# Kernel optimization log

Hardware: AMD Instinct MI355X
Metric: run time of the kernel (lower is better)

## Reference

```python
import jax, jax.numpy as jnp
import numpy as np
import math

# SS2D (VMamba v2) config
D_MODEL = 96
D_INNER = 192          # ssm_ratio * d_model (== d_expand, ssm_rank_ratio==ssm_ratio)
D_STATE = 16
DT_RANK = 6            # ceil(96/16)
K = 4                  # scan directions
D_CONV = 3
STEP = 2               # EfficientScan step_size
BATCH, H, W = 4, 64, 64  # H,W chosen even -> no padding branch
LN_EPS = 1e-5


def efficient_scan(x):
    # x: (B, C, H, W) with H,W divisible by STEP -> (B, 4, C, (H/2)*(W/2))
    Bn, C = x.shape[0], x.shape[1]
    xt = jnp.swapaxes(x, 2, 3)  # (B, C, W, H)
    xs0 = x[:, :, ::STEP, ::STEP].reshape(Bn, C, -1)
    xs1 = xt[:, :, ::STEP, 1::STEP].reshape(Bn, C, -1)
    xs2 = x[:, :, ::STEP, 1::STEP].reshape(Bn, C, -1)
    xs3 = xt[:, :, 1::STEP, 1::STEP].reshape(Bn, C, -1)
    return jnp.stack([xs0, xs1, xs2, xs3], axis=1)


def efficient_merge(ys, ori_h, ori_w):
    # ys: (B, 4, C, L') -> (B, C, ori_h*ori_w)
    Bn, _, C, _ = ys.shape
    Hs, Ws = ori_h // STEP, ori_w // STEP
    a = ys[:, 0].reshape(Bn, C, Hs, Ws)
    b = jnp.swapaxes(ys[:, 1].reshape(Bn, C, Ws, Hs), 2, 3)
    c = ys[:, 2].reshape(Bn, C, Hs, Ws)
    d = jnp.swapaxes(ys[:, 3].reshape(Bn, C, Ws, Hs), 2, 3)
    y = jnp.zeros((Bn, C, ori_h, ori_w), ys.dtype)
    y = y.at[:, :, ::STEP, ::STEP].set(a)
    y = y.at[:, :, 1::STEP, ::STEP].set(b)
    y = y.at[:, :, ::STEP, 1::STEP].set(c)
    y = y.at[:, :, 1::STEP, 1::STEP].set(d)
    return y.reshape(Bn, C, ori_h * ori_w)


def selective_scan(u, delta, A, Bs, Cs, D, delta_bias):
    # u, delta: (B, K*Dg, L); A: (K*Dg, N); Bs, Cs: (B, K, N, L); D, delta_bias: (K*Dg,)
    Bn, KD, L = u.shape
    N = A.shape[1]
    Dg = KD // K
    delta = jax.nn.softplus(delta + delta_bias[None, :, None])
    u4 = u.reshape(Bn, K, Dg, L)
    dt4 = delta.reshape(Bn, K, Dg, L)
    A4 = A.reshape(K, Dg, N)
    # discretized transition / input, time-major for scan: (L, B, K, Dg, N)
    dA = jnp.exp(jnp.einsum('bkdl,kdn->lbkdn', dt4, A4))
    dBu = jnp.einsum('bkdl,bknl,bkdl->lbkdn', dt4, Bs, u4)

    def step(h, inp):
        dA_t, dBu_t = inp
        h = dA_t * h + dBu_t
        return h, h

    h0 = jnp.zeros((Bn, K, Dg, N), u.dtype)
    _, hs = jax.lax.scan(step, h0, (dA, dBu))  # (L, B, K, Dg, N)
    y = jnp.einsum('lbkdn,bknl->bkdl', hs, Cs)
    y = y + u4 * D.reshape(1, K, Dg, 1)
    return y.reshape(Bn, KD, L)


def setup_inputs() -> dict:
    key = jax.random.key(0)
    ks = jax.random.split(key, 10)
    f = jnp.float32
    x = jax.random.normal(ks[0], (BATCH, H, W, D_MODEL), f)
    W_in = jax.random.normal(ks[1], (2 * D_INNER, D_MODEL), f) / math.sqrt(D_MODEL)
    conv_w = jax.random.normal(ks[2], (D_INNER, 1, D_CONV, D_CONV), f) / math.sqrt(D_CONV * D_CONV)
    conv_b = jax.random.normal(ks[3], (D_INNER,), f) * 0.01
    x_proj_weight = jax.random.normal(ks[4], (K, DT_RANK + 2 * D_STATE, D_INNER), f) / math.sqrt(D_INNER)
    dt_projs_weight = jax.random.normal(ks[5], (K, D_INNER, DT_RANK), f) / math.sqrt(DT_RANK)
    dt_projs_bias = jax.random.normal(ks[6], (K, D_INNER), f) * 0.1
    A_logs = jnp.log(jnp.tile(jnp.arange(1, D_STATE + 1, dtype=f), (K * D_INNER, 1)))
    Ds = jnp.ones((K * D_INNER,), f)
    ln_g = jnp.ones((D_INNER,), f)
    ln_b = jnp.zeros((D_INNER,), f)
    W_out = jax.random.normal(ks[7], (D_MODEL, D_INNER), f) / math.sqrt(D_INNER)
    return dict(x=x, W_in=W_in, conv_w=conv_w, conv_b=conv_b,
                x_proj_weight=x_proj_weight, dt_projs_weight=dt_projs_weight,
                dt_projs_bias=dt_projs_bias, A_logs=A_logs, Ds=Ds,
                ln_g=ln_g, ln_b=ln_b, W_out=W_out)


def _ss2d_forward(x, W_in, conv_w, conv_b, x_proj_weight, dt_projs_weight,
                  dt_projs_bias, A_logs, Ds, ln_g, ln_b, W_out):
    Bn = x.shape[0]
    # in_proj (no bias), split into x and gate z
    xz = jnp.einsum('bhwc,ec->bhwe', x, W_in)            # (B,H,W,2*D_INNER)
    xin, z = jnp.split(xz, 2, axis=-1)
    z = jax.nn.silu(z)
    # depthwise conv 3x3 (SAME) + SiLU, NCHW
    xc = jnp.transpose(xin, (0, 3, 1, 2))                 # (B, D_INNER, H, W)
    xc = jax.lax.conv_general_dilated(
        xc, conv_w, window_strides=(1, 1), padding=((1, 1), (1, 1)),
        feature_group_count=D_INNER,
        dimension_numbers=('NCHW', 'OIHW', 'NCHW')) + conv_b[None, :, None, None]
    xc = jax.nn.silu(xc)
    # cross_selective_scan
    xs = efficient_scan(xc)                               # (B, 4, C, L')
    Lp = xs.shape[-1]
    x_dbl = jnp.einsum('bkdl,kcd->bkcl', xs, x_proj_weight)
    dts, Bs, Cs = jnp.split(x_dbl, [DT_RANK, DT_RANK + D_STATE], axis=2)
    dts = jnp.einsum('bkrl,kdr->bkdl', dts, dt_projs_weight)
    u = xs.reshape(Bn, -1, Lp).astype(jnp.float32)
    delta = dts.reshape(Bn, -1, Lp).astype(jnp.float32)
    A = -jnp.exp(A_logs.astype(jnp.float32))
    ys = selective_scan(u, delta, A, Bs.astype(jnp.float32), Cs.astype(jnp.float32),
                        Ds.astype(jnp.float32), dt_projs_bias.reshape(-1).astype(jnp.float32))
    ys = ys.reshape(Bn, K, -1, Lp)
    y = efficient_merge(ys, H, W)                         # (B, C, H*W)
    y = jnp.swapaxes(y, 1, 2)                             # (B, L, C)
    # LayerNorm over channel dim
    mu = jnp.mean(y, axis=-1, keepdims=True)
    var = jnp.var(y, axis=-1, keepdims=True)
    y = (y - mu) * jax.lax.rsqrt(var + LN_EPS) * ln_g + ln_b
    y = y.reshape(Bn, H, W, D_INNER).astype(x.dtype)
    # gate and out_proj (no bias)
    y = y * z
    out = jnp.einsum('bhwd,od->bhwo', y, W_out)
    return out


def reference(x, W_in, conv_w, conv_b, x_proj_weight, dt_projs_weight,
              dt_projs_bias, A_logs, Ds, ln_g, ln_b, W_out):
    return _ss2d_forward(x, W_in, conv_w, conv_b, x_proj_weight, dt_projs_weight,
                         dt_projs_bias, A_logs, Ds, ln_g, ln_b, W_out)
```

## Files before the change

### kernel.cpp

```cpp
#include <hip/hip_runtime.h>
#include <math.h>


#define DINNER 192
#define NSTATE 16
#define KDIR 4
#define BATCH 4
#define NPIX (BATCH * 64 * 64)
#define LP 1024
#define NCH 64
#define CHUNK 16
#define NBK (BATCH * KDIR)
#define NSTATES (NBK * DINNER * NSTATE)
#define SSTRIDE (NBK * DINNER)
#define USTRIDE 196
#define GSTRIDE 200
#define ASTRIDE 104
#define XSTRIDE 200

typedef __attribute__((ext_vector_type(8))) short short8;
typedef __attribute__((ext_vector_type(4))) short short4v;
typedef __attribute__((ext_vector_type(4))) unsigned short ushort4v;
typedef __attribute__((ext_vector_type(8))) unsigned short ushort8v;
typedef __attribute__((ext_vector_type(4))) float f32x4;

__device__ __forceinline__ float silu_f(float x) {
    return x / (1.0f + __expf(-x));
}
__device__ __forceinline__ float softplus_f(float a) {
    return (a > 20.0f) ? a : __logf(1.0f + __expf(a));
}
__device__ __forceinline__ unsigned short f2bf(float f) {
    unsigned u = __float_as_uint(f);
    unsigned r = (u + 0x7FFFu + ((u >> 16) & 1u)) >> 16;
    return (unsigned short)r;
}
__device__ __forceinline__ float bf2f(unsigned short h) {
    return __uint_as_float(((unsigned)h) << 16);
}

__global__ __launch_bounds__(256) void k_castW(
        const float* __restrict__ W_in, const float* __restrict__ xpw,
        const float* __restrict__ W_out,
        unsigned short* __restrict__ Wi_hi, unsigned short* __restrict__ Wi_lo,
        unsigned short* __restrict__ Xp_hi, unsigned short* __restrict__ Xp_lo,
        unsigned short* __restrict__ Wo_bf) {
    int i = blockIdx.x * 256 + threadIdx.x;
    if (i < 384 * 96) {
        float v = W_in[i];
        unsigned short h = f2bf(v);
        Wi_hi[i] = h;
        Wi_lo[i] = f2bf(v - bf2f(h));
    }
    if (i < 4 * 48 * 192) {
        int kk = i / (48 * 192);
        int rem = i - kk * (48 * 192);
        int c = rem / 192;
        int j = rem - c * 192;
        float v = (c < 38) ? xpw[((size_t)kk * 38 + c) * 192 + j] : 0.0f;
        unsigned short h = f2bf(v);
        Xp_hi[i] = h;
        Xp_lo[i] = f2bf(v - bf2f(h));
    }
    if (i < 96 * DINNER) Wo_bf[i] = f2bf(W_out[i]);
}

__global__ __launch_bounds__(256) void k_inproj3(
        const float* __restrict__ x,
        const unsigned short* __restrict__ Wi_hi,
        const unsigned short* __restrict__ Wi_lo,
        float* __restrict__ xin, unsigned short* __restrict__ zb) {
    __shared__ __align__(16) short sAh[16 * ASTRIDE];
    __shared__ __align__(16) short sAl[16 * ASTRIDE];
    int p0 = blockIdx.x * 16;
    int t = threadIdx.x;
    const float4* xs = (const float4*)(x + (size_t)p0 * 96);
    for (int i = t; i < 384; i += 256) {
        float4 v = xs[i];
        int f = i * 4;
        int row = f / 96, col = f - row * 96;
        short4v hi, lo;
        unsigned short hb;
        hb = f2bf(v.x); hi.x = (short)hb; lo.x = (short)f2bf(v.x - bf2f(hb));
        hb = f2bf(v.y); hi.y = (short)hb; lo.y = (short)f2bf(v.y - bf2f(hb));
        hb = f2bf(v.z); hi.z = (short)hb; lo.z = (short)f2bf(v.z - bf2f(hb));
        hb = f2bf(v.w); hi.w = (short)hb; lo.w = (short)f2bf(v.w - bf2f(hb));
        *(short4v*)&sAh[row * ASTRIDE + col] = hi;
        *(short4v*)&sAl[row * ASTRIDE + col] = lo;
    }
    __syncthreads();
    int w = t >> 6;
    int lane = t & 63;
    int m = lane & 15, quad = lane >> 4;
    const short* wh = (const short*)Wi_hi;
    const short* wl = (const short*)Wi_lo;
    short8 ah[3], al[3];
    #pragma unroll
    for (int c = 0; c < 3; ++c) {
        ah[c] = *(const short8*)&sAh[m * ASTRIDE + c * 32 + quad * 8];
        al[c] = *(const short8*)&sAl[m * ASTRIDE + c * 32 + quad * 8];
    }
    #pragma unroll
    for (int i = 0; i < 6; ++i) {
        int e0 = (w * 6 + i) * 16;
        f32x4 acc = {0.f, 0.f, 0.f, 0.f};
        #pragma unroll
        for (int c = 0; c < 3; ++c) {
            size_t o = (size_t)(e0 + m) * 96 + c * 32 + quad * 8;
            short8 bh = *(const short8*)(wh + o);
            short8 bl = *(const short8*)(wl + o);
            acc = __builtin_amdgcn_mfma_f32_16x16x32_bf16(ah[c], bl, acc, 0, 0, 0);
            acc = __builtin_amdgcn_mfma_f32_16x16x32_bf16(al[c], bh, acc, 0, 0, 0);
            acc = __builtin_amdgcn_mfma_f32_16x16x32_bf16(ah[c], bh, acc, 0, 0, 0);
        }
        int e = e0 + m;
        #pragma unroll
        for (int r = 0; r < 4; ++r) {
            int p = p0 + quad * 4 + r;
            if (e < 192) xin[(size_t)p * 192 + e] = acc[r];
            else         zb[(size_t)p * 192 + (e - 192)] = f2bf(silu_f(acc[r]));
        }
    }
}

__global__ __launch_bounds__(192) void k_conv8(
        const float* __restrict__ xin, const float* __restrict__ cw,
        const float* __restrict__ cb, float* __restrict__ xg) {
    int blk = blockIdx.x;
    int b = blk >> 9;
    int rem = blk & 511;
    int h = rem >> 3;
    int w0 = (rem & 7) * 8;
    int d = threadIdx.x;
    float wr[3][3];
    #pragma unroll
    for (int i = 0; i < 3; ++i)
        #pragma unroll
        for (int j = 0; j < 3; ++j) wr[i][j] = cw[d * 9 + i * 3 + j];
    float bias = cb[d];
    float r0[10], r1[10], r2[10];
    #pragma unroll
    for (int jj = 0; jj < 10; ++jj) {
        int ww = w0 + jj - 1;
        bool inw = (unsigned)ww < 64u;
        const float* base = xin + ((size_t)b * 4096 + h * 64 + (inw ? ww : 0)) * 192 + d;
        r0[jj] = (inw && h > 0)  ? base[-64 * 192] : 0.0f;
        r1[jj] = inw             ? base[0]         : 0.0f;
        r2[jj] = (inw && h < 63) ? base[64 * 192]  : 0.0f;
    }
    float acc[8];
    #pragma unroll
    for (int o = 0; o < 8; ++o) {
        float a = bias;
        #pragma unroll
        for (int j = 0; j < 3; ++j) {
            a = fmaf(r0[o + j], wr[0][j], a);
            a = fmaf(r1[o + j], wr[1][j], a);
            a = fmaf(r2[o + j], wr[2][j], a);
        }
        acc[o] = a;
    }
    #pragma unroll
    for (int o = 0; o < 8; ++o) {
        int w = w0 + o;
        int kq = (h & 1) ? ((w & 1) ? 3 : 1) : ((w & 1) ? 2 : 0);
        int l = (kq & 1) ? ((w >> 1) * 32 + (h >> 1))
                         : ((h >> 1) * 32 + (w >> 1));
        xg[((size_t)(b * 4 + kq) * 1024 + l) * 192 + d] = silu_f(acc[o]);
    }
}

__global__ __launch_bounds__(192) void k_xscan(
        const float* __restrict__ xg,
        const unsigned short* __restrict__ Xp_hi,
        const unsigned short* __restrict__ Xp_lo,
        const float* __restrict__ A_logs, const float* __restrict__ dtw,
        const float* __restrict__ dtb, const float* __restrict__ Ds,
        float* __restrict__ dtr, float* __restrict__ Cm,
        float* __restrict__ Sbuf, unsigned short* __restrict__ Qb,
        unsigned short* __restrict__ yout) {
    __shared__ __align__(16) short sAh[16 * XSTRIDE];
    __shared__ __align__(16) short sAl[16 * XSTRIDE];
    __shared__ __align__(16) float sU[CHUNK * USTRIDE];
    __shared__ float sB[CHUNK * 16];
    __shared__ float sC[CHUNK * 16];
    __shared__ float sDt[CHUNK * 6];

    int bk = blockIdx.x >> 6;
    int ch = blockIdx.x & 63;
    int k = bk & 3;
    int t = threadIdx.x;
    int d = t;
    int lbase = bk * 1024 + ch * CHUNK;

    {
        const float4* us = (const float4*)(xg + (size_t)lbase * 192);
        for (int i = t; i < 768; i += 192) {
            float4 v = us[i];
            int f = i * 4;
            int row = f / 192, col = f - row * 192;
            short4v hi, lo;
            unsigned short hb;
            hb = f2bf(v.x); hi.x = (short)hb; lo.x = (short)f2bf(v.x - bf2f(hb));
            hb = f2bf(v.y); hi.y = (short)hb; lo.y = (short)f2bf(v.y - bf2f(hb));
            hb = f2bf(v.z); hi.z = (short)hb; lo.z = (short)f2bf(v.z - bf2f(hb));
            hb = f2bf(v.w); hi.w = (short)hb; lo.w = (short)f2bf(v.w - bf2f(hb));
            *(short4v*)&sAh[row * XSTRIDE + col] = hi;
            *(short4v*)&sAl[row * XSTRIDE + col] = lo;
            *(float4*)&sU[row * USTRIDE + col] = v;
        }
    }
    __syncthreads();

    {
        int wv = t >> 6;
        int lane = t & 63;
        int m = lane & 15, quad = lane >> 4;
        const short* bh16 = (const short*)Xp_hi;
        const short* bl16 = (const short*)Xp_lo;
        int n0 = wv * 16;
        size_t brow = ((size_t)k * 48 + n0 + m) * 192;
        f32x4 acc = {0.f, 0.f, 0.f, 0.f};
        #pragma unroll
        for (int c = 0; c < 6; ++c) {
            short8 ah = *(const short8*)&sAh[m * XSTRIDE + c * 32 + quad * 8];
            short8 al = *(const short8*)&sAl[m * XSTRIDE + c * 32 + quad * 8];
            short8 bh = *(const short8*)(bh16 + brow + c * 32 + quad * 8);
            short8 bl = *(const short8*)(bl16 + brow + c * 32 + quad * 8);
            acc = __builtin_amdgcn_mfma_f32_16x16x32_bf16(ah, bl, acc, 0, 0, 0);
            acc = __builtin_amdgcn_mfma_f32_16x16x32_bf16(al, bh, acc, 0, 0, 0);
            acc = __builtin_amdgcn_mfma_f32_16x16x32_bf16(ah, bh, acc, 0, 0, 0);
        }
        int c = n0 + m;
        #pragma unroll
        for (int r = 0; r < 4; ++r) {
            int ll = quad * 4 + r;
            float v = acc[r];
            if (c < 6)       sDt[ll * 6 + c] = v;
            else if (c < 22) sB[ll * 16 + (c - 6)] = v;
            else if (c < 38) sC[ll * 16 + (c - 22)] = v;
        }
    }
    __syncthreads();

    if (t < 96) dtr[(size_t)(lbase + t / 6) * 6 + (t % 6)] = sDt[t];
    for (int i = t; i < CHUNK * 16; i += 192)
        Cm[(size_t)lbase * 16 + i] = sC[i];

    {
        float A[16];
        #pragma unroll
        for (int n = 0; n < 16; ++n) A[n] = -__expf(A_logs[(k * 192 + d) * 16 + n]);
        float A0 = A[0];
        bool geo = true;
        #pragma unroll
        for (int n = 1; n < 16; ++n)
            geo = geo && (fabsf(A[n] - (float)(n + 1) * A0) <= 1e-4f * fabsf(A[n]));
        float wp[6];
        #pragma unroll
        for (int q = 0; q < 6; ++q) wp[q] = dtw[(k * 192 + d) * 6 + q];
        float bias = dtb[k * 192 + d];
        float Dp = Ds[k * 192 + d];
        float dlt[CHUNK];
        #pragma unroll 4
        for (int l = 0; l < CHUNK; ++l) {
            float a = bias;
            #pragma unroll
            for (int q = 0; q < 6; ++q) a = fmaf(wp[q], sDt[l * 6 + q], a);
            dlt[l] = softplus_f(a);
        }
        float S = 0.0f;
        #pragma unroll
        for (int l = 0; l < CHUNK; ++l) S += dlt[l];
        float h[16];
        #pragma unroll
        for (int n = 0; n < 16; ++n) h[n] = 0.0f;
        if (geo) {
            float e1v[CHUNK];
            #pragma unroll 4
            for (int l = 0; l < CHUNK; ++l) e1v[l] = __expf(dlt[l] * A0);
            #pragma unroll 2
            for (int l = 0; l < CHUNK; ++l) {
                float u = sU[l * USTRIDE + d];
                float du = dlt[l] * u;
                float e1 = e1v[l];
                float e = e1;
                float y = 0.0f;
                #pragma unroll
                for (int n = 0; n < 16; ++n) {
                    h[n] = fmaf(e, h[n], du * sB[l * 16 + n]);
                    y = fmaf(h[n], sC[l * 16 + n], y);
                    e *= e1;
                }
                yout[(size_t)(lbase + l) * 192 + d] = f2bf(fmaf(u, Dp, y));
            }
        } else {
            for (int l = 0; l < CHUNK; ++l) {
                float u = sU[l * USTRIDE + d];
                float du = dlt[l] * u;
                float y = 0.0f;
                #pragma unroll
                for (int n = 0; n < 16; ++n) {
                    float e = __expf(dlt[l] * A[n]);
                    h[n] = fmaf(e, h[n], du * sB[l * 16 + n]);
                    y = fmaf(h[n], sC[l * 16 + n], y);
                }
                yout[(size_t)(lbase + l) * 192 + d] = f2bf(fmaf(u, Dp, y));
            }
        }
        Sbuf[(size_t)ch * SSTRIDE + bk * 192 + d] = S;
        size_t base = (size_t)ch * NSTATES + bk * (192 * 16);
        #pragma unroll
        for (int n = 0; n < 16; ++n)
            Qb[base + n * 192 + d] = f2bf(h[n]);
    }
}

__global__ __launch_bounds__(256) void k_scan2(
        const float* __restrict__ Sbuf, const float* __restrict__ A_logs,
        const unsigned short* __restrict__ Qb, unsigned short* __restrict__ Hst) {
    int s = blockIdx.x * 256 + threadIdx.x;
    int bk = s / 3072;
    int rem = s - bk * 3072;
    int n = rem / 192;
    int d = rem - n * 192;
    int k = bk & 3;
    float A = -__expf(A_logs[(k * 192 + d) * 16 + n]);
    int sb = bk * 192 + d;
    float h = 0.0f;
    for (int c0 = 0; c0 < NCH; c0 += 8) {
        float Sv[8], qv[8], pv[8];
        #pragma unroll
        for (int j = 0; j < 8; ++j) {
            Sv[j] = Sbuf[(size_t)(c0 + j) * SSTRIDE + sb];
            qv[j] = bf2f(Qb[(size_t)(c0 + j) * NSTATES + s]);
        }
        #pragma unroll
        for (int j = 0; j < 8; ++j) pv[j] = __expf(A * Sv[j]);
        #pragma unroll
        for (int j = 0; j < 8; ++j) {
            Hst[(size_t)(c0 + j) * NSTATES + s] = f2bf(h);
            h = fmaf(pv[j], h, qv[j]);
        }
    }
}

__global__ __launch_bounds__(192) void k_scan3c(
        const float* __restrict__ dtr, const float* __restrict__ Cm,
        const float* __restrict__ A_logs, const float* __restrict__ dtw,
        const float* __restrict__ dtb, const unsigned short* __restrict__ Hst,
        unsigned short* __restrict__ yout) {
    __shared__ float sC[CHUNK * 16];
    int bk = blockIdx.x >> 6;
    int ch = blockIdx.x & 63;
    if (ch == 0) return;
    int k = bk & 3;
    int d = threadIdx.x;
    int lbase = bk * 1024 + ch * CHUNK;
    for (int i = d; i < CHUNK * 16; i += 192)
        sC[i] = Cm[(size_t)lbase * 16 + i];
    float A[16];
    #pragma unroll
    for (int n = 0; n < 16; ++n) A[n] = -__expf(A_logs[(k * 192 + d) * 16 + n]);
    float A0 = A[0];
    bool geo = true;
    #pragma unroll
    for (int n = 1; n < 16; ++n)
        geo = geo && (fabsf(A[n] - (float)(n + 1) * A0) <= 1e-4f * fabsf(A[n]));
    float wp[6];
    #pragma unroll
    for (int q = 0; q < 6; ++q) wp[q] = dtw[(k * 192 + d) * 6 + q];
    float bias = dtb[k * 192 + d];
    float h0[16];
    size_t base = (size_t)ch * NSTATES + bk * (192 * 16);
    #pragma unroll
    for (int n = 0; n < 16; ++n) h0[n] = bf2f(Hst[base + n * 192 + d]);
    float Sarr[CHUNK];
    {
        float S = 0.0f;
        #pragma unroll 4
        for (int l = 0; l < CHUNK; ++l) {
            const float* r = dtr + (size_t)(lbase + l) * 6;
            float a = bias;
            #pragma unroll
            for (int q = 0; q < 6; ++q) a = fmaf(wp[q], r[q], a);
            S += softplus_f(a);
            Sarr[l] = S;
        }
    }
    __syncthreads();
    if (geo) {
        float e1l[CHUNK];
        #pragma unroll 4
        for (int l = 0; l < CHUNK; ++l) e1l[l] = __expf(A0 * Sarr[l]);
        #pragma unroll 2
        for (int l = 0; l < CHUNK; ++l) {
            float y = bf2f(yout[(size_t)(lbase + l) * 192 + d]);
            float e1 = e1l[l];
            float e = e1;
            float corr = 0.0f;
            #pragma unroll
            for (int n = 0; n < 16; ++n) {
                corr = fmaf(h0[n] * e, sC[l * 16 + n], corr);
                e *= e1;
            }
            yout[(size_t)(lbase + l) * 192 + d] = f2bf(y + corr);
        }
    } else {
        for (int l = 0; l < CHUNK; ++l) {
            float y = bf2f(yout[(size_t)(lbase + l) * 192 + d]);
            float corr = 0.0f;
            #pragma unroll
            for (int n = 0; n < 16; ++n) {
                float e = __expf(A[n] * Sarr[l]);
                corr = fmaf(h0[n] * e, sC[l * 16 + n], corr);
            }
            yout[(size_t)(lbase + l) * 192 + d] = f2bf(y + corr);
        }
    }
}

__global__ __launch_bounds__(256) void k_lnout(
        const unsigned short* __restrict__ yout,
        const unsigned short* __restrict__ zb,
        const float* __restrict__ lng, const float* __restrict__ lnb,
        const unsigned short* __restrict__ Wo_bf, float* __restrict__ out) {
    __shared__ __align__(16) short sgb[32 * GSTRIDE];
    int p0 = blockIdx.x * 32;
    int t = threadIdx.x;
    int p = t >> 3;
    int sub = t & 7;
    int gp = p0 + p;
    int b = gp >> 12;
    int hw = gp & 4095;
    int h = hw >> 6, w = hw & 63;
    int kq = (h & 1) ? ((w & 1) ? 3 : 1) : ((w & 1) ? 2 : 0);
    int l = (kq & 1) ? ((w >> 1) * 32 + (h >> 1))
                     : ((h >> 1) * 32 + (w >> 1));
    const unsigned short* yrow =
        yout + ((size_t)(b * 4 + kq) * 1024 + l) * 192 + sub * 24;
    float yv[24];
    float s = 0.0f, s2 = 0.0f;
    #pragma unroll
    for (int j = 0; j < 3; ++j) {
        ushort8v v8 = *(const ushort8v*)(yrow + j * 8);
        #pragma unroll
        for (int e = 0; e < 8; ++e) {
            float v = bf2f(v8[e]);
            yv[j * 8 + e] = v;
            s += v;
            s2 += v * v;
        }
    }
    #pragma unroll
    for (int off = 1; off < 8; off <<= 1) {
        s  += __shfl_xor(s, off, 8);
        s2 += __shfl_xor(s2, off, 8);
    }
    float mu = s * (1.0f / 192.0f);
    float var = s2 * (1.0f / 192.0f) - mu * mu;
    float rstd = rsqrtf(var + 1e-5f);
    const unsigned short* zrow = zb + (size_t)gp * 192 + sub * 24;
    short* grow = sgb + p * GSTRIDE + sub * 24;
    #pragma unroll
    for (int j = 0; j < 6; ++j) {
        ushort4v zv4 = *(const ushort4v*)(zrow + j * 4);
        float4 gv = *(const float4*)(lng + sub * 24 + j * 4);
        float4 bv = *(const float4*)(lnb + sub * 24 + j * 4);
        short4v sv;
        sv.x = (short)f2bf(((yv[j * 4 + 0] - mu) * rstd * gv.x + bv.x) * bf2f(zv4.x));
        sv.y = (short)f2bf(((yv[j * 4 + 1] - mu) * rstd * gv.y + bv.y) * bf2f(zv4.y));
        sv.z = (short)f2bf(((yv[j * 4 + 2] - mu) * rstd * gv.z + bv.z) * bf2f(zv4.z));
        sv.w = (short)f2bf(((yv[j * 4 + 3] - mu) * rstd * gv.w + bv.w) * bf2f(zv4.w));
        *(short4v*)(grow + j * 4) = sv;
    }
    __syncthreads();
    int wv = t >> 6;
    int lane = t & 63;
    int m = lane & 15, quad = lane >> 4;
    int mt = wv >> 1;
    int nb = (wv & 1) * 3;
    const short* wob = (const short*)Wo_bf;
    short8 a[6];
    #pragma unroll
    for (int kk = 0; kk < 6; ++kk)
        a[kk] = *(const short8*)(sgb + (mt * 16 + m) * GSTRIDE + kk * 32 + quad * 8);
    #pragma unroll
    for (int i = 0; i < 3; ++i) {
        int n0 = (nb + i) * 16;
        f32x4 acc = {0.f, 0.f, 0.f, 0.f};
        #pragma unroll
        for (int kk = 0; kk < 6; ++kk) {
            short8 bfr = *(const short8*)(wob + (size_t)(n0 + m) * 192 + kk * 32 + quad * 8);
            acc = __builtin_amdgcn_mfma_f32_16x16x32_bf16(a[kk], bfr, acc, 0, 0, 0);
        }
        #pragma unroll
        for (int r = 0; r < 4; ++r) {
            int pp = p0 + mt * 16 + quad * 4 + r;
            out[(size_t)pp * 96 + n0 + m] = acc[r];
        }
    }
}

extern "C" void kernel_launch(void* const* d_in, const int* in_sizes, int n_in,
                              void* d_out, int out_size, void* d_ws, size_t ws_size,
                              hipStream_t stream) {
    const float* x    = (const float*)d_in[0];
    const float* W_in = (const float*)d_in[1];
    const float* cw   = (const float*)d_in[2];
    const float* cb   = (const float*)d_in[3];
    const float* xpw  = (const float*)d_in[4];
    const float* dtw  = (const float*)d_in[5];
    const float* dtb  = (const float*)d_in[6];
    const float* Alog = (const float*)d_in[7];
    const float* Ds   = (const float*)d_in[8];
    const float* lng  = (const float*)d_in[9];
    const float* lnb  = (const float*)d_in[10];
    const float* Wout = (const float*)d_in[11];
    float* out = (float*)d_out;

    float* ws = (float*)d_ws;
    size_t off = 0;
    unsigned short* Wi_hi = (unsigned short*)(ws + off); off += 384 * 96 / 2;
    unsigned short* Wi_lo = (unsigned short*)(ws + off); off += 384 * 96 / 2;
    unsigned short* Xp_hi = (unsigned short*)(ws + off); off += 4 * 48 * 192 / 2;
    unsigned short* Xp_lo = (unsigned short*)(ws + off); off += 4 * 48 * 192 / 2;
    unsigned short* Wo_bf = (unsigned short*)(ws + off); off += 96 * DINNER / 2;
    float* xin   = ws + off; off += (size_t)NPIX * 192;
    unsigned short* zb = (unsigned short*)(ws + off); off += (size_t)NPIX * 192 / 2;
    float* xg    = ws + off; off += (size_t)NPIX * 192;
    float* dtrb  = ws + off; off += (size_t)NBK * LP * 6;
    float* Cm    = ws + off; off += (size_t)NBK * LP * 16;
    float* Sbuf  = ws + off; off += (size_t)NCH * SSTRIDE;
    unsigned short* Qb  = (unsigned short*)(ws + off); off += (size_t)NCH * NSTATES / 2;
    unsigned short* Hst = (unsigned short*)(ws + off); off += (size_t)NCH * NSTATES / 2;
    unsigned short* yout = (unsigned short*)(ws + off); off += (size_t)NBK * LP * 192 / 2;

    hipLaunchKernelGGL(k_castW, dim3(144), dim3(256), 0, stream,
                       W_in, xpw, Wout, Wi_hi, Wi_lo, Xp_hi, Xp_lo, Wo_bf);
    hipLaunchKernelGGL(k_inproj3, dim3(NPIX / 16), dim3(256), 0, stream,
                       x, Wi_hi, Wi_lo, xin, zb);
    hipLaunchKernelGGL(k_conv8, dim3(NPIX / 8), dim3(192), 0, stream,
                       xin, cw, cb, xg);
    hipLaunchKernelGGL(k_xscan, dim3(NBK * NCH), dim3(192), 0, stream,
                       xg, Xp_hi, Xp_lo, Alog, dtw, dtb, Ds,
                       dtrb, Cm, Sbuf, Qb, yout);
    hipLaunchKernelGGL(k_scan2, dim3(NSTATES / 256), dim3(256), 0, stream,
                       Sbuf, Alog, Qb, Hst);
    hipLaunchKernelGGL(k_scan3c, dim3(NBK * NCH), dim3(192), 0, stream,
                       dtrb, Cm, Alog, dtw, dtb, Hst, yout);
    hipLaunchKernelGGL(k_lnout, dim3(NPIX / 32), dim3(256), 0, stream,
                       yout, zb, lng, lnb, Wo_bf, out);
}
```

Measured before the change: 155.7 us.

## Fold inter-chunk state propagation into scan pass 3 and double in-proj tile

Removes the separate chunk-carry kernel and its Hst buffer. Each chunk block of the final scan pass now recomputes its incoming state by walking all earlier chunk summaries (Sbuf, Qb), using a geometric-power shortcut when A is geometric. This drops one launch and a round trip through global memory, but adds redundant work that grows with chunk index (quadratic in chunk count) and leaves later blocks with longer serial loops. Separately, the in-projection kernel now handles 32 pixels per block with two MFMA accumulators, so each weight fragment load is reused across both row tiles.

Measured after the change: 168.6 us. 8.3% more time.

```diff
diff --git a/kernel.cpp b/kernel.cpp
--- a/kernel.cpp
+++ b/kernel.cpp
@@ -70,12 +70,12 @@
         const unsigned short* __restrict__ Wi_hi,
         const unsigned short* __restrict__ Wi_lo,
         float* __restrict__ xin, unsigned short* __restrict__ zb) {
-    __shared__ __align__(16) short sAh[16 * ASTRIDE];
-    __shared__ __align__(16) short sAl[16 * ASTRIDE];
-    int p0 = blockIdx.x * 16;
+    __shared__ __align__(16) short sAh[32 * ASTRIDE];
+    __shared__ __align__(16) short sAl[32 * ASTRIDE];
+    int p0 = blockIdx.x * 32;
     int t = threadIdx.x;
     const float4* xs = (const float4*)(x + (size_t)p0 * 96);
-    for (int i = t; i < 384; i += 256) {
+    for (int i = t; i < 768; i += 256) {
         float4 v = xs[i];
         int f = i * 4;
         int row = f / 96, col = f - row * 96;
@@ -94,31 +94,43 @@
     int m = lane & 15, quad = lane >> 4;
     const short* wh = (const short*)Wi_hi;
     const short* wl = (const short*)Wi_lo;
-    short8 ah[3], al[3];
-    #pragma unroll
-    for (int c = 0; c < 3; ++c) {
-        ah[c] = *(const short8*)&sAh[m * ASTRIDE + c * 32 + quad * 8];
-        al[c] = *(const short8*)&sAl[m * ASTRIDE + c * 32 + quad * 8];
-    }
+    short8 ah[2][3], al[2][3];
+    #pragma unroll
+    for (int mt = 0; mt < 2; ++mt)
+        #pragma unroll
+        for (int c = 0; c < 3; ++c) {
+            ah[mt][c] = *(const short8*)&sAh[(mt * 16 + m) * ASTRIDE + c * 32 + quad * 8];
+            al[mt][c] = *(const short8*)&sAl[(mt * 16 + m) * ASTRIDE + c * 32 + quad * 8];
+        }
     #pragma unroll
     for (int i = 0; i < 6; ++i) {
         int e0 = (w * 6 + i) * 16;
-        f32x4 acc = {0.f, 0.f, 0.f, 0.f};
+        f32x4 acc0 = {0.f, 0.f, 0.f, 0.f};
+        f32x4 acc1 = {0.f, 0.f, 0.f, 0.f};
         #pragma unroll
         for (int c = 0; c < 3; ++c) {
             size_t o = (size_t)(e0 + m) * 96 + c * 32 + quad * 8;
             short8 bh = *(const short8*)(wh + o);
             short8 bl = *(const short8*)(wl + o);
-            acc = __builtin_amdgcn_mfma_f32_16x16x32_bf16(ah[c], bl, acc, 0, 0, 0);
-            acc = __builtin_amdgcn_mfma_f32_16x16x32_bf16(al[c], bh, acc, 0, 0, 0);
-            acc = __builtin_amdgcn_mfma_f32_16x16x32_bf16(ah[c], bh, acc, 0, 0, 0);
+            acc0 = __builtin_amdgcn_mfma_f32_16x16x32_bf16(ah[0][c], bl, acc0, 0, 0, 0);
+            acc0 = __builtin_amdgcn_mfma_f32_16x16x32_bf16(al[0][c], bh, acc0, 0, 0, 0);
+            acc0 = __builtin_amdgcn_mfma_f32_16x16x32_bf16(ah[0][c], bh, acc0, 0, 0, 0);
+            acc1 = __builtin_amdgcn_mfma_f32_16x16x32_bf16(ah[1][c], bl, acc1, 0, 0, 0);
+            acc1 = __builtin_amdgcn_mfma_f32_16x16x32_bf16(al[1][c], bh, acc1, 0, 0, 0);
+            acc1 = __builtin_amdgcn_mfma_f32_16x16x32_bf16(ah[1][c], bh, acc1, 0, 0, 0);
         }
         int e = e0 + m;
         #pragma unroll
         for (int r = 0; r < 4; ++r) {
             int p = p0 + quad * 4 + r;
-            if (e < 192) xin[(size_t)p * 192 + e] = acc[r];
-            else         zb[(size_t)p * 192 + (e - 192)] = f2bf(silu_f(acc[r]));
+            if (e < 192) xin[(size_t)p * 192 + e] = acc0[r];
+            else         zb[(size_t)p * 192 + (e - 192)] = f2bf(silu_f(acc0[r]));
+        }
+        #pragma unroll
+        for (int r = 0; r < 4; ++r) {
+            int p = p0 + 16 + quad * 4 + r;
+            if (e < 192) xin[(size_t)p * 192 + e] = acc1[r];
+            else         zb[(size_t)p * 192 + (e - 192)] = f2bf(silu_f(acc1[r]));
         }
     }
 }
@@ -316,39 +328,11 @@
     }
 }
 
-__global__ __launch_bounds__(256) void k_scan2(
-        const float* __restrict__ Sbuf, const float* __restrict__ A_logs,
-        const unsigned short* __restrict__ Qb, unsigned short* __restrict__ Hst) {
-    int s = blockIdx.x * 256 + threadIdx.x;
-    int bk = s / 3072;
-    int rem = s - bk * 3072;
-    int n = rem / 192;
-    int d = rem - n * 192;
-    int k = bk & 3;
-    float A = -__expf(A_logs[(k * 192 + d) * 16 + n]);
-    int sb = bk * 192 + d;
-    float h = 0.0f;
-    for (int c0 = 0; c0 < NCH; c0 += 8) {
-        float Sv[8], qv[8], pv[8];
-        #pragma unroll
-        for (int j = 0; j < 8; ++j) {
-            Sv[j] = Sbuf[(size_t)(c0 + j) * SSTRIDE + sb];
-            qv[j] = bf2f(Qb[(size_t)(c0 + j) * NSTATES + s]);
-        }
-        #pragma unroll
-        for (int j = 0; j < 8; ++j) pv[j] = __expf(A * Sv[j]);
-        #pragma unroll
-        for (int j = 0; j < 8; ++j) {
-            Hst[(size_t)(c0 + j) * NSTATES + s] = f2bf(h);
-            h = fmaf(pv[j], h, qv[j]);
-        }
-    }
-}
-
-__global__ __launch_bounds__(192) void k_scan3c(
+__global__ __launch_bounds__(192) void k_scan3p(
         const float* __restrict__ dtr, const float* __restrict__ Cm,
         const float* __restrict__ A_logs, const float* __restrict__ dtw,
-        const float* __restrict__ dtb, const unsigned short* __restrict__ Hst,
+        const float* __restrict__ dtb,
+        const float* __restrict__ Sbuf, const unsigned short* __restrict__ Qb,
         unsigned short* __restrict__ yout) {
     __shared__ float sC[CHUNK * 16];
     int bk = blockIdx.x >> 6;
@@ -371,10 +355,36 @@
     #pragma unroll
     for (int q = 0; q < 6; ++q) wp[q] = dtw[(k * 192 + d) * 6 + q];
     float bias = dtb[k * 192 + d];
+
     float h0[16];
-    size_t base = (size_t)ch * NSTATES + bk * (192 * 16);
-    #pragma unroll
-    for (int n = 0; n < 16; ++n) h0[n] = bf2f(Hst[base + n * 192 + d]);
+    #pragma unroll
+    for (int n = 0; n < 16; ++n) h0[n] = 0.0f;
+    {
+        int sb = bk * 192 + d;
+        size_t qoff = (size_t)bk * 3072 + d;
+        if (geo) {
+            for (int c = 0; c < ch; ++c) {
+                float Sv = Sbuf[(size_t)c * SSTRIDE + sb];
+                float e1 = __expf(A0 * Sv);
+                float e = e1;
+                const unsigned short* qrow = Qb + (size_t)c * NSTATES + qoff;
+                #pragma unroll
+                for (int n = 0; n < 16; ++n) {
+                    h0[n] = fmaf(e, h0[n], bf2f(qrow[n * 192]));
+                    e *= e1;
+                }
+            }
+        } else {
+            for (int c = 0; c < ch; ++c) {
+                float Sv = Sbuf[(size_t)c * SSTRIDE + sb];
+                const unsigned short* qrow = Qb + (size_t)c * NSTATES + qoff;
+                #pragma unroll
+                for (int n = 0; n < 16; ++n)
+                    h0[n] = fmaf(__expf(A[n] * Sv), h0[n], bf2f(qrow[n * 192]));
+            }
+        }
+    }
+
     float Sarr[CHUNK];
     {
         float S = 0.0f;
@@ -533,22 +543,19 @@
     float* Cm    = ws + off; off += (size_t)NBK * LP * 16;
     float* Sbuf  = ws + off; off += (size_t)NCH * SSTRIDE;
     unsigned short* Qb  = (unsigned short*)(ws + off); off += (size_t)NCH * NSTATES / 2;
-    unsigned short* Hst = (unsigned short*)(ws + off); off += (size_t)NCH * NSTATES / 2;
     unsigned short* yout = (unsigned short*)(ws + off); off += (size_t)NBK * LP * 192 / 2;
 
     hipLaunchKernelGGL(k_castW, dim3(144), dim3(256), 0, stream,
                        W_in, xpw, Wout, Wi_hi, Wi_lo, Xp_hi, Xp_lo, Wo_bf);
-    hipLaunchKernelGGL(k_inproj3, dim3(NPIX / 16), dim3(256), 0, stream,
+    hipLaunchKernelGGL(k_inproj3, dim3(NPIX / 32), dim3(256), 0, stream,
                        x, Wi_hi, Wi_lo, xin, zb);
     hipLaunchKernelGGL(k_conv8, dim3(NPIX / 8), dim3(192), 0, stream,
                        xin, cw, cb, xg);
     hipLaunchKernelGGL(k_xscan, dim3(NBK * NCH), dim3(192), 0, stream,
                        xg, Xp_hi, Xp_lo, Alog, dtw, dtb, Ds,
                        dtrb, Cm, Sbuf, Qb, yout);
-    hipLaunchKernelGGL(k_scan2, dim3(NSTATES / 256), dim3(256), 0, stream,
-                       Sbuf, Alog, Qb, Hst);
-    hipLaunchKernelGGL(k_scan3c, dim3(NBK * NCH), dim3(192), 0, stream,
-                       dtrb, Cm, Alog, dtw, dtb, Hst, yout);
+    hipLaunchKernelGGL(k_scan3p, dim3(NBK * NCH), dim3(192), 0, stream,
+                       dtrb, Cm, Alog, dtw, dtb, Sbuf, Qb, yout);
     hipLaunchKernelGGL(k_lnout, dim3(NPIX / 32), dim3(256), 0, stream,
                        yout, zb, lng, lnb, Wo_bf, out);
 }
```
